# Optimization experiments

Hardware: AMD Instinct MI355X
Metric: run time of the kernel (lower is better)

The kernel has to match this reference:

```python
import jax, jax.numpy as jnp
import numpy as np

B = 2048          # batch_size from init
D = 512           # embedding dim
TAU = 0.5         # temperature
EPS = 1e-12       # torch F.normalize eps


def _l2_normalize(x):
    n = jnp.linalg.norm(x, axis=1, keepdims=True)
    return x / jnp.maximum(n, EPS)


def setup_inputs() -> dict:
    key = jax.random.key(0)
    k1, k2 = jax.random.split(key)
    emb_i = jax.random.normal(k1, (2 * B, D), dtype=jnp.float32)
    emb_j = jax.random.normal(k2, (2 * B, D), dtype=jnp.float32)
    return {"emb_i": emb_i, "emb_j": emb_j}


def reference(emb_i, emb_j):
    z_i = _l2_normalize(emb_i)
    z_j = _l2_normalize(emb_j)
    rep = jnp.concatenate([z_i, z_j], axis=0)        # [4B, D], unit rows
    # cosine similarity of unit vectors == plain GEMM
    sim = rep @ rep.T                                # [4B, 4B]
    n = 4 * B
    pos1 = jnp.concatenate([jnp.diagonal(sim, B), jnp.diagonal(sim, -B)])        # [6B]
    pos2 = jnp.concatenate([jnp.diagonal(sim, 2 * B), jnp.diagonal(sim, -2 * B)])  # [4B]
    pos3 = jnp.concatenate([jnp.diagonal(sim, 3 * B), jnp.diagonal(sim, -3 * B)])  # [2B]
    nominator = (jnp.sum(jnp.exp(pos1 / TAU))
                 + jnp.sum(jnp.exp(pos2 / TAU))
                 + jnp.sum(jnp.exp(pos3 / TAU)))
    off_diag = 1.0 - jnp.eye(n, dtype=sim.dtype)
    denominator = jnp.sum(off_diag * jnp.exp(sim / TAU)) - nominator
    loss = -jnp.log(nominator / denominator) / (4 * B)
    return loss
```

## Files before the change

### kernel.cpp

```cpp
#include <hip/hip_runtime.h>
#include <stdint.h>

#define DIM       512
#define NROWS     8192
#define HALF_ROWS 4096
#define TILE      128
#define BKP       64
#define NTILE     64
#define NBLK      2080

typedef float  floatx4 __attribute__((ext_vector_type(4)));
typedef __bf16 bf16x8  __attribute__((ext_vector_type(8)));

__device__ __forceinline__ void async_copy16(const unsigned short* g, unsigned short* l) {
    __builtin_amdgcn_global_load_lds(
        (const __attribute__((address_space(1))) uint32_t*)(g),
        (__attribute__((address_space(3))) uint32_t*)(l),
        16, 0, 0);
}

__global__ __launch_bounds__(256) void normalize_kernel(
    const float* __restrict__ emb_i, const float* __restrict__ emb_j,
    unsigned short* __restrict__ rep, double* __restrict__ ws)
{
    if (blockIdx.x == 0 && threadIdx.x == 0) {
        ws[0] = 0.0;
        ws[1] = 0.0;
        *(unsigned int*)((char*)ws + 16) = 0u;
    }
    const int wave = threadIdx.x >> 6;
    const int lane = threadIdx.x & 63;
    const int row  = blockIdx.x * 4 + wave;
    const float* src = (row < HALF_ROWS) ? (emb_i + (size_t)row * DIM)
                                         : (emb_j + (size_t)(row - HALF_ROWS) * DIM);
    const int c = lane * 8;
    float4 v0 = *(const float4*)(src + c);
    float4 v1 = *(const float4*)(src + c + 4);
    float s = v0.x*v0.x + v0.y*v0.y + v0.z*v0.z + v0.w*v0.w
            + v1.x*v1.x + v1.y*v1.y + v1.z*v1.z + v1.w*v1.w;
    #pragma unroll
    for (int off = 32; off; off >>= 1) s += __shfl_xor(s, off, 64);
    const float nrm = sqrtf(s);
    const float inv = 1.0f / fmaxf(nrm, 1e-12f);
    float f[8] = {v0.x*inv, v0.y*inv, v0.z*inv, v0.w*inv,
                  v1.x*inv, v1.y*inv, v1.z*inv, v1.w*inv};
    union { unsigned short h[8]; uint4 u; } pk;
    #pragma unroll
    for (int t = 0; t < 8; ++t) {
        uint32_t b = __float_as_uint(f[t]);
        b += 0x7FFFu + ((b >> 16) & 1u);
        pk.h[t] = (unsigned short)(b >> 16);
    }
    *(uint4*)(rep + (size_t)row * DIM + c) = pk.u;
}

__global__ __launch_bounds__(256) void gram_kernel(
    const unsigned short* __restrict__ rep, double* __restrict__ ws,
    float* __restrict__ out)
{
    int s = blockIdx.x >> 6;
    int Bi = 0, rem = s;
    while (rem >= 8 - Bi) { rem -= 8 - Bi; ++Bi; }
    const int Bj = Bi + rem;
    const int t = blockIdx.x & 63;
    const int bi = Bi * 8 + (t >> 3);
    const int bj = Bj * 8 + (t & 7);
    if (bi > bj) return;

    __shared__ unsigned short As[TILE * BKP];
    __shared__ unsigned short Bs[TILE * BKP];
    __shared__ float red[8];

    const int tid  = threadIdx.x;
    const int wave = tid >> 6, lane = tid & 63;
    const int wm = wave >> 1, wn = wave & 1;
    const int m = lane & 15, quad = lane >> 4;
    const int sw0 = ((quad)     ^ (m & 7)) * 8;
    const int sw1 = ((4 + quad) ^ (m & 7)) * 8;

    floatx4 acc[4][4];
    #pragma unroll
    for (int a = 0; a < 4; ++a)
        #pragma unroll
        for (int b = 0; b < 4; ++b)
            #pragma unroll
            for (int e = 0; e < 4; ++e) acc[a][b][e] = 0.0f;

    const int i0 = bi * TILE, j0 = bj * TILE;

    int rr[4], jj[4];
    #pragma unroll
    for (int q = 0; q < 4; ++q) {
        const int p = q * 256 + tid;
        rr[q] = p >> 3;
        jj[q] = ((p & 7) ^ (rr[q] & 7)) * 8;
    }

    for (int k0 = 0; k0 < DIM; k0 += BKP) {
        #pragma unroll
        for (int q = 0; q < 4; ++q) {
            const int p = q * 256 + tid;
            async_copy16(rep + (size_t)(i0 + rr[q]) * DIM + k0 + jj[q], As + p * 8);
            async_copy16(rep + (size_t)(j0 + rr[q]) * DIM + k0 + jj[q], Bs + p * 8);
        }
        __syncthreads();

        #pragma unroll
        for (int kk = 0; kk < 2; ++kk) {
            const int sw = kk ? sw1 : sw0;
            bf16x8 af[4], bfr[4];
            #pragma unroll
            for (int mt = 0; mt < 4; ++mt)
                af[mt] = *(const bf16x8*)(As + (wm * 64 + mt * 16 + m) * BKP + sw);
            #pragma unroll
            for (int nt = 0; nt < 4; ++nt)
                bfr[nt] = *(const bf16x8*)(Bs + (wn * 64 + nt * 16 + m) * BKP + sw);
            #pragma unroll
            for (int mt = 0; mt < 4; ++mt)
                #pragma unroll
                for (int nt = 0; nt < 4; ++nt)
                    acc[mt][nt] = __builtin_amdgcn_mfma_f32_16x16x32_bf16(
                        af[mt], bfr[nt], acc[mt][nt], 0, 0, 0);
        }
        __syncthreads();
    }

    float s_all = 0.0f, s_pos = 0.0f;
    const float LOG2E2 = 2.885390081777927f;
    #pragma unroll
    for (int mt = 0; mt < 4; ++mt) {
        const int ibase = i0 + wm * 64 + mt * 16 + quad * 4;
        #pragma unroll
        for (int nt = 0; nt < 4; ++nt) {
            const int j = j0 + wn * 64 + nt * 16 + m;
            const floatx4 a = acc[mt][nt];
            #pragma unroll
            for (int r2 = 0; r2 < 4; ++r2) {
                const int i = ibase + r2;
                const float e = exp2f(a[r2] * LOG2E2);
                if (i != j) s_all += e;
                const int d = j - i;
                if (d == 2048 || d == 4096 || d == 6144) s_pos += e;
            }
        }
    }
    #pragma unroll
    for (int off = 32; off; off >>= 1) {
        s_all += __shfl_xor(s_all, off, 64);
        s_pos += __shfl_xor(s_pos, off, 64);
    }
    if (lane == 0) { red[wave] = s_all; red[4 + wave] = s_pos; }
    __syncthreads();
    if (tid == 0) {
        const float w  = (bi == bj) ? 1.0f : 2.0f;
        const double ta = (double)((red[0] + red[1] + red[2] + red[3]) * w);
        const double tp = (double)((red[4] + red[5] + red[6] + red[7]) * w);
        const double r0 = atomicAdd(&ws[0], ta);
        const double r1 = atomicAdd(&ws[1], tp);
        const unsigned dep =
            (unsigned)(((unsigned long long)__double_as_longlong(r0) >> 63) &
                       ((unsigned long long)__double_as_longlong(r1) >> 63));
        unsigned int* cnt = (unsigned int*)((char*)ws + 16);
        const unsigned int prev = atomicAdd(cnt, 1u + dep);
        if (prev == NBLK - 1) {
            const double tot = atomicAdd(&ws[0], 0.0);
            const double nom = atomicAdd(&ws[1], 0.0);
            const double den = tot - nom;
            out[0] = (float)(-log(nom / den) / (double)NROWS);
        }
    }
}

extern "C" void kernel_launch(void* const* d_in, const int* in_sizes, int n_in,
                              void* d_out, int out_size, void* d_ws, size_t ws_size,
                              hipStream_t stream) {
    const float* emb_i = (const float*)d_in[0];
    const float* emb_j = (const float*)d_in[1];
    float* out = (float*)d_out;
    double* ws = (double*)d_ws;
    unsigned short* rep = (unsigned short*)((char*)d_ws + 256);

    hipLaunchKernelGGL(normalize_kernel, dim3(NROWS / 4), dim3(256), 0, stream,
                       emb_i, emb_j, rep, ws);
    hipLaunchKernelGGL(gram_kernel, dim3(36 * 64), dim3(256), 0, stream, rep, ws, out);
}
```

Baseline: 163.2 us.

## Pre-swizzle rep into MFMA fragment layout and load operands directly from global

Result: slower. 180.6 us (+10.6%).

```diff
diff --git a/kernel.cpp b/kernel.cpp
--- a/kernel.cpp
+++ b/kernel.cpp
@@ -5,19 +5,12 @@
 #define NROWS     8192
 #define HALF_ROWS 4096
 #define TILE      128
-#define BKP       64
 #define NTILE     64
 #define NBLK      2080
 
 typedef float  floatx4 __attribute__((ext_vector_type(4)));
 typedef __bf16 bf16x8  __attribute__((ext_vector_type(8)));
 
-__device__ __forceinline__ void async_copy16(const unsigned short* g, unsigned short* l) {
-    __builtin_amdgcn_global_load_lds(
-        (const __attribute__((address_space(1))) uint32_t*)(g),
-        (__attribute__((address_space(3))) uint32_t*)(l),
-        16, 0, 0);
-}
 
 __global__ __launch_bounds__(256) void normalize_kernel(
     const float* __restrict__ emb_i, const float* __restrict__ emb_j,
@@ -51,10 +44,11 @@
         b += 0x7FFFu + ((b >> 16) & 1u);
         pk.h[t] = (unsigned short)(b >> 16);
     }
-    *(uint4*)(rep + (size_t)row * DIM + c) = pk.u;
+    const size_t pg = (size_t)((row >> 4) * 16 + (lane >> 2)) * 512;
+    *(uint4*)(rep + pg + ((lane & 3) * 16 + (row & 15)) * 8) = pk.u;
 }
 
-__global__ __launch_bounds__(256) void gram_kernel(
+__global__ __launch_bounds__(256, 3) void gram_kernel(
     const unsigned short* __restrict__ rep, double* __restrict__ ws,
     float* __restrict__ out)
 {
@@ -67,16 +61,12 @@
     const int bj = Bj * 8 + (t & 7);
     if (bi > bj) return;
 
-    __shared__ unsigned short As[TILE * BKP];
-    __shared__ unsigned short Bs[TILE * BKP];
     __shared__ float red[8];
 
     const int tid  = threadIdx.x;
     const int wave = tid >> 6, lane = tid & 63;
     const int wm = wave >> 1, wn = wave & 1;
     const int m = lane & 15, quad = lane >> 4;
-    const int sw0 = ((quad)     ^ (m & 7)) * 8;
-    const int sw1 = ((4 + quad) ^ (m & 7)) * 8;
 
     floatx4 acc[4][4];
     #pragma unroll
@@ -88,41 +78,42 @@
 
     const int i0 = bi * TILE, j0 = bj * TILE;
 
-    int rr[4], jj[4];
+    const unsigned short* aP = rep + (size_t)((i0 >> 4) + wm * 4) * 8192 + lane * 8;
+    const unsigned short* bP = rep + (size_t)((j0 >> 4) + wn * 4) * 8192 + lane * 8;
+
+    bf16x8 a0[4], b0[4], a1[4], b1[4];
     #pragma unroll
-    for (int q = 0; q < 4; ++q) {
-        const int p = q * 256 + tid;
-        rr[q] = p >> 3;
-        jj[q] = ((p & 7) ^ (rr[q] & 7)) * 8;
+    for (int mt = 0; mt < 4; ++mt) {
+        a0[mt] = *(const bf16x8*)(aP + mt * 8192);
+        b0[mt] = *(const bf16x8*)(bP + mt * 8192);
     }
 
-    for (int k0 = 0; k0 < DIM; k0 += BKP) {
+    #pragma unroll 1
+    for (int kc = 0; kc < 16; kc += 2) {
+        const int k1 = kc + 1;
+        const int k2 = (kc + 2 < 16) ? kc + 2 : 15;
         #pragma unroll
-        for (int q = 0; q < 4; ++q) {
-            const int p = q * 256 + tid;
-            async_copy16(rep + (size_t)(i0 + rr[q]) * DIM + k0 + jj[q], As + p * 8);
-            async_copy16(rep + (size_t)(j0 + rr[q]) * DIM + k0 + jj[q], Bs + p * 8);
+        for (int mt = 0; mt < 4; ++mt) {
+            a1[mt] = *(const bf16x8*)(aP + k1 * 512 + mt * 8192);
+            b1[mt] = *(const bf16x8*)(bP + k1 * 512 + mt * 8192);
         }
-        __syncthreads();
-
         #pragma unroll
-        for (int kk = 0; kk < 2; ++kk) {
-            const int sw = kk ? sw1 : sw0;
-            bf16x8 af[4], bfr[4];
-            #pragma unroll
-            for (int mt = 0; mt < 4; ++mt)
-                af[mt] = *(const bf16x8*)(As + (wm * 64 + mt * 16 + m) * BKP + sw);
+        for (int mt = 0; mt < 4; ++mt)
             #pragma unroll
             for (int nt = 0; nt < 4; ++nt)
-                bfr[nt] = *(const bf16x8*)(Bs + (wn * 64 + nt * 16 + m) * BKP + sw);
+                acc[mt][nt] = __builtin_amdgcn_mfma_f32_16x16x32_bf16(
+                    a0[mt], b0[nt], acc[mt][nt], 0, 0, 0);
+        #pragma unroll
+        for (int mt = 0; mt < 4; ++mt) {
+            a0[mt] = *(const bf16x8*)(aP + k2 * 512 + mt * 8192);
+            b0[mt] = *(const bf16x8*)(bP + k2 * 512 + mt * 8192);
+        }
+        #pragma unroll
+        for (int mt = 0; mt < 4; ++mt)
             #pragma unroll
-            for (int mt = 0; mt < 4; ++mt)
-                #pragma unroll
-                for (int nt = 0; nt < 4; ++nt)
-                    acc[mt][nt] = __builtin_amdgcn_mfma_f32_16x16x32_bf16(
-                        af[mt], bfr[nt], acc[mt][nt], 0, 0, 0);
-        }
-        __syncthreads();
+            for (int nt = 0; nt < 4; ++nt)
+                acc[mt][nt] = __builtin_amdgcn_mfma_f32_16x16x32_bf16(
+                    a1[mt], b1[nt], acc[mt][nt], 0, 0, 0);
     }
 
     float s_all = 0.0f, s_pos = 0.0f;
```

## Store normalized rep in MFMA-fragment-packed layout and shrink K-chunk to 32

Applied to the files above, without the earlier changes.

Measured after the change: 159.6 us. 1.02x faster.

```diff
diff --git a/kernel.cpp b/kernel.cpp
--- a/kernel.cpp
+++ b/kernel.cpp
@@ -5,12 +5,12 @@
 #define NROWS     8192
 #define HALF_ROWS 4096
 #define TILE      128
-#define BKP       64
 #define NTILE     64
 #define NBLK      2080
 
 typedef float  floatx4 __attribute__((ext_vector_type(4)));
 typedef __bf16 bf16x8  __attribute__((ext_vector_type(8)));
+
 
 __device__ __forceinline__ void async_copy16(const unsigned short* g, unsigned short* l) {
     __builtin_amdgcn_global_load_lds(
@@ -51,10 +51,11 @@
         b += 0x7FFFu + ((b >> 16) & 1u);
         pk.h[t] = (unsigned short)(b >> 16);
     }
-    *(uint4*)(rep + (size_t)row * DIM + c) = pk.u;
+    const size_t pg = (size_t)((row >> 4) * 16 + (lane >> 2)) * 512;
+    *(uint4*)(rep + pg + ((lane & 3) * 16 + (row & 15)) * 8) = pk.u;
 }
 
-__global__ __launch_bounds__(256) void gram_kernel(
+__global__ __launch_bounds__(256, 3) void gram_kernel(
     const unsigned short* __restrict__ rep, double* __restrict__ ws,
     float* __restrict__ out)
 {
@@ -67,16 +68,14 @@
     const int bj = Bj * 8 + (t & 7);
     if (bi > bj) return;
 
-    __shared__ unsigned short As[TILE * BKP];
-    __shared__ unsigned short Bs[TILE * BKP];
+    __shared__ unsigned short As[TILE * 32];
+    __shared__ unsigned short Bs[TILE * 32];
     __shared__ float red[8];
 
     const int tid  = threadIdx.x;
     const int wave = tid >> 6, lane = tid & 63;
     const int wm = wave >> 1, wn = wave & 1;
     const int m = lane & 15, quad = lane >> 4;
-    const int sw0 = ((quad)     ^ (m & 7)) * 8;
-    const int sw1 = ((4 + quad) ^ (m & 7)) * 8;
 
     floatx4 acc[4][4];
     #pragma unroll
@@ -87,41 +86,37 @@
             for (int e = 0; e < 4; ++e) acc[a][b][e] = 0.0f;
 
     const int i0 = bi * TILE, j0 = bj * TILE;
+    const unsigned short* aSrc0 = rep + ((size_t)(bi * 128 + 16 * (0 * 4 + wave))) * 512 + lane * 8;
+    const unsigned short* aSrc1 = rep + ((size_t)(bi * 128 + 16 * (1 * 4 + wave))) * 512 + lane * 8;
+    const unsigned short* bSrc0 = rep + ((size_t)(bj * 128 + 16 * (0 * 4 + wave))) * 512 + lane * 8;
+    const unsigned short* bSrc1 = rep + ((size_t)(bj * 128 + 16 * (1 * 4 + wave))) * 512 + lane * 8;
+    unsigned short* aDst0 = As + (size_t)(0 * 256 + tid) * 8;
+    unsigned short* aDst1 = As + (size_t)(1 * 256 + tid) * 8;
+    unsigned short* bDst0 = Bs + (size_t)(0 * 256 + tid) * 8;
+    unsigned short* bDst1 = Bs + (size_t)(1 * 256 + tid) * 8;
 
-    int rr[4], jj[4];
-    #pragma unroll
-    for (int q = 0; q < 4; ++q) {
-        const int p = q * 256 + tid;
-        rr[q] = p >> 3;
-        jj[q] = ((p & 7) ^ (rr[q] & 7)) * 8;
-    }
+    const unsigned short* aFrag = As + (size_t)(wm * 4) * 512 + lane * 8;
+    const unsigned short* bFrag = Bs + (size_t)(wn * 4) * 512 + lane * 8;
 
-    for (int k0 = 0; k0 < DIM; k0 += BKP) {
-        #pragma unroll
-        for (int q = 0; q < 4; ++q) {
-            const int p = q * 256 + tid;
-            async_copy16(rep + (size_t)(i0 + rr[q]) * DIM + k0 + jj[q], As + p * 8);
-            async_copy16(rep + (size_t)(j0 + rr[q]) * DIM + k0 + jj[q], Bs + p * 8);
-        }
+    for (int kc = 0; kc < 16; ++kc) {
+        async_copy16(aSrc0 + kc * 512, aDst0);
+        async_copy16(bSrc0 + kc * 512, bDst0);
+        async_copy16(aSrc1 + kc * 512, aDst1);
+        async_copy16(bSrc1 + kc * 512, bDst1);
         __syncthreads();
 
+        bf16x8 af[4], bfr[4];
         #pragma unroll
-        for (int kk = 0; kk < 2; ++kk) {
-            const int sw = kk ? sw1 : sw0;
-            bf16x8 af[4], bfr[4];
-            #pragma unroll
-            for (int mt = 0; mt < 4; ++mt)
-                af[mt] = *(const bf16x8*)(As + (wm * 64 + mt * 16 + m) * BKP + sw);
+        for (int mt = 0; mt < 4; ++mt) {
+            af[mt]  = *(const bf16x8*)(aFrag + mt * 512);
+            bfr[mt] = *(const bf16x8*)(bFrag + mt * 512);
+        }
+        #pragma unroll
+        for (int mt = 0; mt < 4; ++mt)
             #pragma unroll
             for (int nt = 0; nt < 4; ++nt)
-                bfr[nt] = *(const bf16x8*)(Bs + (wn * 64 + nt * 16 + m) * BKP + sw);
-            #pragma unroll
-            for (int mt = 0; mt < 4; ++mt)
-                #pragma unroll
-                for (int nt = 0; nt < 4; ++nt)
-                    acc[mt][nt] = __builtin_amdgcn_mfma_f32_16x16x32_bf16(
-                        af[mt], bfr[nt], acc[mt][nt], 0, 0, 0);
-        }
+                acc[mt][nt] = __builtin_amdgcn_mfma_f32_16x16x32_bf16(
+                    af[mt], bfr[nt], acc[mt][nt], 0, 0, 0);
         __syncthreads();
     }
 
```
